# Kernel optimization log

Hardware: AMD Instinct MI355X
Metric: run time of the kernel (lower is better)

## Reference

```python
import jax, jax.numpy as jnp
import numpy as np

NO = 16          # config['Max_Object']
NT = 8           # config['Max_Time']
FEAT = 512       # config['feat_dims']
VIS_IN = 2048
TGT = 24


def setup_inputs() -> dict:
    key = jax.random.key(0)
    ks = jax.random.split(key, 10)
    b = 16
    N = NT * 2 * NO  # 256
    s = lambda k, *sh: jax.random.normal(k, sh, dtype=jnp.float32) * 0.02
    return {
        "src": jax.random.normal(ks[0], (b, 1, 1, N, VIS_IN), dtype=jnp.float32),
        "tgt_rel": jax.random.randint(ks[1], (b * NT * NO * NO,), 0, TGT, dtype=jnp.int64),
        "w1": s(ks[2], VIS_IN, FEAT), "b1": jnp.zeros((FEAT,), jnp.float32),
        "w2": s(ks[3], FEAT, FEAT),   "b2": jnp.zeros((FEAT,), jnp.float32),
        "wf": s(ks[4], FEAT, FEAT),   "bf": jnp.zeros((FEAT,), jnp.float32),
        "wr": s(ks[5], 2 * FEAT, TGT), "br": jnp.zeros((TGT,), jnp.float32),
    }


def reference(src, tgt_rel, w1, b1, w2, b2, wf, bf, wr, br):
    b = src.shape[0]
    BT = b * NT
    # src[:, 0, 0, :, :] -> (b, N, D) -> (b*NT, 2*NO, D); take visual part [:2048]
    x = src[:, 0, 0, :, :].reshape(BT, 2 * NO, -1)[:, :, :VIS_IN]
    # fc_vis: MLP 2048 -> FEAT -> FEAT
    h = jnp.maximum(x @ w1 + b1, 0.0) @ w2 + b2          # (BT, 2NO, FEAT)
    node_feats = h @ wf + bf                             # fc_fusion
    # vectorized replacement of the NOxNO python double loop:
    # edge[:, i*NO + (j-NO), :] = cat(node[:, i], node[:, j])  for i<NO<=j
    subj = jnp.broadcast_to(node_feats[:, :NO, None, :], (BT, NO, NO, FEAT))
    obj = jnp.broadcast_to(node_feats[:, None, NO:, :], (BT, NO, NO, FEAT))
    edge_feats = jnp.concatenate([subj, obj], axis=-1).reshape(BT, NO * NO, 2 * FEAT)
    out = (edge_feats @ wr + br).reshape(-1, TGT)        # fc_rel
    tgt = tgt_rel.reshape(-1)
    w_cls = jnp.asarray([1.0] + [100.0] * (TGT - 1), dtype=out.dtype)
    logp = jax.nn.log_softmax(out, axis=-1)
    nll = -jnp.take_along_axis(logp, tgt[:, None], axis=1)[:, 0]
    ww = w_cls[tgt]
    loss = jnp.sum(ww * nll) / jnp.sum(ww)  # torch weighted cross_entropy (mean)
    return out, tgt, loss
```

## Files before the change

### kernel.cpp

```cpp
#include <hip/hip_runtime.h>
#include <cstddef>
#include <cstdint>

#define NOBJ   16
#define FEAT   512
#define VIS    2048
#define NTGT   24
#define MROWS  4096
#define EROWS  32768

typedef __attribute__((ext_vector_type(8))) short short8;
typedef __attribute__((ext_vector_type(4))) float f32x4;
typedef __attribute__((ext_vector_type(16))) float f32x16;

__device__ __forceinline__ unsigned short f2bf(float f) {
    union { float f; unsigned int i; } v; v.f = f;
    const unsigned int x = v.i;
    return (unsigned short)((x + 0x7fffu + ((x >> 16) & 1u)) >> 16);
}

__device__ __forceinline__ void gload16(const unsigned short* g, unsigned short* l) {
    __builtin_amdgcn_global_load_lds(
        (const __attribute__((address_space(1))) unsigned int*)(const void*)g,
        (__attribute__((address_space(3))) unsigned int*)(void*)l, 16, 0, 0);
}

__global__ __launch_bounds__(256)
void prep1(const float* __restrict__ w1, unsigned short* __restrict__ w1t,
           const float* __restrict__ wf, const float* __restrict__ bfv,
           const float* __restrict__ wr, float* __restrict__ t1,
           const float* __restrict__ src, unsigned short* __restrict__ srcb,
           float* __restrict__ P) {
    __shared__ float shbuf[FEAT * NTGT];
    const int b   = blockIdx.x;
    const int tid = threadIdx.x;
    if (b < 1024) {
        float (*tile)[33] = (float(*)[33])shbuf;
        const int k0 = (b & 63) * 32;
        const int n0 = (b >> 6) * 32;
        const int tx = tid & 31, ty = tid >> 5;
        #pragma unroll
        for (int r = 0; r < 32; r += 8)
            tile[ty + r][tx] = w1[(size_t)(k0 + ty + r) * FEAT + n0 + tx];
        __syncthreads();
        #pragma unroll
        for (int r = 0; r < 32; r += 8)
            w1t[(size_t)(n0 + ty + r) * VIS + k0 + tx] = f2bf(tile[tx][ty + r]);
    } else if (b < 1050) {
        const int bb = b - 1024;
        const int h  = bb / 13, blk = bb % 13;
        const float* wrh = wr + (size_t)h * FEAT * NTGT;
        for (int idx = tid; idx < FEAT * NTGT; idx += 256)
            shbuf[idx] = wrh[idx];
        __syncthreads();
        if (tid < 252) {
            const int krow = blk * 42 + tid / 6;
            const int cg   = tid % 6;
            if (krow <= 512) {
                const float* rowp = (krow < 512) ? (wf + (size_t)krow * FEAT) : bfv;
                const f32x4* shb4 = (const f32x4*)shbuf;
                f32x4 p = {0.f, 0.f, 0.f, 0.f};
                #pragma unroll 4
                for (int j = 0; j < FEAT; j += 4) {
                    const float4 a = *reinterpret_cast<const float4*>(rowp + j);
                    const f32x4 w0 = shb4[(j + 0) * 6 + cg];
                    const f32x4 w1v = shb4[(j + 1) * 6 + cg];
                    const f32x4 w2v = shb4[(j + 2) * 6 + cg];
                    const f32x4 w3v = shb4[(j + 3) * 6 + cg];
                    p += a.x * w0 + a.y * w1v + a.z * w2v + a.w * w3v;
                }
                *reinterpret_cast<f32x4*>(t1 + ((size_t)h * 513 + krow) * 32 + cg * 4) = p;
            }
        }
    } else if (b < 2074) {
        const int bb = b - 1050;
        #pragma unroll
        for (int q = 0; q < 4; ++q) {
            const size_t i = (size_t)bb * 8192 + q * 2048 + tid * 8;
            const float4 a = *reinterpret_cast<const float4*>(src + i);
            const float4 c = *reinterpret_cast<const float4*>(src + i + 4);
            short8 o;
            o[0] = (short)f2bf(a.x); o[1] = (short)f2bf(a.y);
            o[2] = (short)f2bf(a.z); o[3] = (short)f2bf(a.w);
            o[4] = (short)f2bf(c.x); o[5] = (short)f2bf(c.y);
            o[6] = (short)f2bf(c.z); o[7] = (short)f2bf(c.w);
            *reinterpret_cast<short8*>(srcb + i) = o;
        }
    } else {
        const int bb = b - 2074;
        P[(size_t)bb * 256 + tid] = 0.f;
    }
}

__global__ __launch_bounds__(256)
void prep2(const float* __restrict__ w2, const float* __restrict__ b2,
           const float* __restrict__ t1, unsigned short* __restrict__ wABt,
           float* __restrict__ biasAB) {
    __shared__ float shbuf[FEAT * NTGT];
    const int b   = blockIdx.x;
    const int tid = threadIdx.x;
    const int h   = b / 13, blk = b % 13;
    for (int idx = tid; idx < FEAT * NTGT; idx += 256) {
        const int row = idx / NTGT, col = idx - row * NTGT;
        shbuf[idx] = t1[((size_t)h * 513 + row) * 32 + col];
    }
    __syncthreads();
    if (tid >= 252) return;
    const int r  = blk * 42 + tid / 6;
    const int cg = tid % 6;
    if (r > 512) return;
    const float* rowp = (r < 512) ? (w2 + (size_t)r * FEAT) : b2;
    const f32x4* shb4 = (const f32x4*)shbuf;
    f32x4 p = {0.f, 0.f, 0.f, 0.f};
    #pragma unroll 4
    for (int k = 0; k < FEAT; k += 4) {
        const float4 a = *reinterpret_cast<const float4*>(rowp + k);
        const f32x4 w0 = shb4[(k + 0) * 6 + cg];
        const f32x4 w1v = shb4[(k + 1) * 6 + cg];
        const f32x4 w2v = shb4[(k + 2) * 6 + cg];
        const f32x4 w3v = shb4[(k + 3) * 6 + cg];
        p += a.x * w0 + a.y * w1v + a.z * w2v + a.w * w3v;
    }
    #pragma unroll
    for (int e = 0; e < 4; ++e) {
        const int q = h * NTGT + cg * 4 + e;
        if (r < 512) wABt[(size_t)q * FEAT + r] = f2bf(p[e]);
        else         biasAB[q] = p[e] + t1[((size_t)h * 513 + 512) * 32 + cg * 4 + e];
    }
}

__global__ __launch_bounds__(256)
void gemm1f(const unsigned short* __restrict__ srcb, const unsigned short* __restrict__ w1t,
            const float* __restrict__ b1, const unsigned short* __restrict__ wABt,
            float* __restrict__ P) {
    __shared__ __align__(16) unsigned short As[3][128 * 64];
    __shared__ __align__(16) unsigned short Bs[3][32 * 64];

    const int bid = blockIdx.x;
    const int xcd = bid & 7;
    const int k8  = bid >> 3;
    const int xb  = k8 & 15;
    const int yb  = (xcd << 2) | (k8 >> 4);
    const int m0 = yb * 128;
    const int n0 = xb * 32;

    const int tid  = threadIdx.x;
    const int lane = tid & 63;
    const int wid  = tid >> 6;

    const int aRow = tid >> 3, aCd = (tid & 7) ^ (aRow & 7);
    const int bN   = tid >> 3, bCd = (tid & 7) ^ (bN & 7);
    const size_t aOff = (size_t)(m0 + aRow) * VIS + (aCd << 3);
    const size_t bOff = (size_t)(n0 + bN) * VIS + (bCd << 3);
    const int ldsWb = (wid * 64) << 3;

    f32x16 acc = {};

    #define STAGE(tt, bi)                                                        \
        do {                                                                     \
            const int kn_ = (tt) * 64;                                           \
            _Pragma("unroll")                                                    \
            for (int q_ = 0; q_ < 4; ++q_)                                       \
                gload16(srcb + aOff + (size_t)q_ * 32 * VIS + kn_,               \
                        &As[bi][(q_ * 256) * 8 + ldsWb]);                        \
            gload16(w1t + bOff + kn_, &Bs[bi][ldsWb]);                           \
        } while (0)

    STAGE(0, 0);
    STAGE(1, 1);

    const int NT = VIS / 64;
    for (int t = 0; t < NT; ++t) {
        if (t < NT - 1) asm volatile("s_waitcnt vmcnt(5)" ::: "memory");
        else            asm volatile("s_waitcnt vmcnt(0)" ::: "memory");
        __builtin_amdgcn_s_barrier();
        asm volatile("" ::: "memory");
        if (t + 2 < NT) STAGE(t + 2, (t + 2) % 3);
        const int cb = t % 3;
        #pragma unroll
        for (int k2 = 0; k2 < 4; ++k2) {
            const int chunk = (k2 << 1) + (lane >> 5);
            short8 af, bf8;
            {
                const int row = wid * 32 + (lane & 31);
                const int cw  = chunk ^ (row & 7);
                af = *reinterpret_cast<const short8*>(&As[cb][(row << 6) + (cw << 3)]);
            }
            {
                const int n  = lane & 31;
                const int cw = chunk ^ (n & 7);
                bf8 = *reinterpret_cast<const short8*>(&Bs[cb][(n << 6) + (cw << 3)]);
            }
            acc = __builtin_amdgcn_mfma_f32_32x32x16_bf16(af, bf8, acc, 0, 0, 0);
        }
    }
    #undef STAGE

    unsigned short* Ht = &As[0][0];
    {
        const float bias = b1[n0 + (lane & 31)];
        #pragma unroll
        for (int r = 0; r < 16; ++r) {
            const int row = wid * 32 + (r & 3) + ((r >> 2) << 3) + ((lane >> 5) << 2);
            const float v = fmaxf(acc[r] + bias, 0.f);
            Ht[row * 40 + (lane & 31)] = f2bf(v);
        }
    }
    __syncthreads();

    short8 bq[3];
    #pragma unroll
    for (int t3 = 0; t3 < 3; ++t3)
        bq[t3] = *reinterpret_cast<const short8*>(
            wABt + (size_t)(t3 * 16 + (lane & 15)) * FEAT + n0 + ((lane >> 4) << 3));

    const f32x4 pz = {0.f, 0.f, 0.f, 0.f};
    #pragma unroll
    for (int fr = 0; fr < 2; ++fr) {
        short8 aep;
        {
            const int m = wid * 32 + fr * 16 + (lane & 15);
            aep = *reinterpret_cast<const short8*>(&Ht[m * 40 + ((lane >> 4) << 3)]);
        }
        #pragma unroll
        for (int t3 = 0; t3 < 3; ++t3) {
            f32x4 pp = __builtin_amdgcn_mfma_f32_16x16x32_bf16(aep, bq[t3], pz, 0, 0, 0);
            const int q  = t3 * 16 + (lane & 15);
            const int mb = m0 + wid * 32 + fr * 16 + ((lane >> 4) << 2);
            #pragma unroll
            for (int r = 0; r < 4; ++r)
                atomicAdd(&P[(size_t)(mb + r) * 64 + q], pp[r]);
        }
    }
}

__global__ __launch_bounds__(256)
void out_loss_kernel(const float* __restrict__ P, const float* __restrict__ br,
                     const float* __restrict__ biasAB, const int* __restrict__ tgt,
                     float* __restrict__ out, float* __restrict__ out_tgt,
                     float* __restrict__ partials) {
    __shared__ float sm[32][49];
    const int bt  = blockIdx.x;
    const int tid = threadIdx.x;
    for (int idx = tid; idx < 32 * 48; idx += 256) {
        const int row = idx / 48, col = idx - row * 48;
        sm[row][col] = P[(size_t)(bt * 32 + row) * 64 + col];
    }
    __syncthreads();

    const int r  = bt * 256 + tid;
    const int i  = tid >> 4, j = tid & 15;
    const int tg = tgt[r];

    float vals[NTGT];
    float mx = -1e30f, vtg = 0.f;
    #pragma unroll
    for (int t = 0; t < NTGT; ++t) {
        const float cv = br[t] + biasAB[t] + biasAB[24 + t];
        const float v  = sm[i][t] + sm[16 + j][24 + t] + cv;
        vals[t] = v;
        mx = fmaxf(mx, v);
        if (t == tg) vtg = v;
    }
    float se = 0.f;
    #pragma unroll
    for (int t = 0; t < NTGT; ++t) se += expf(vals[t] - mx);
    const float lse = mx + logf(se);

    float4* o4 = reinterpret_cast<float4*>(out + (size_t)r * NTGT);
    #pragma unroll
    for (int q = 0; q < 6; ++q)
        o4[q] = make_float4(vals[q * 4], vals[q * 4 + 1], vals[q * 4 + 2], vals[q * 4 + 3]);
    out_tgt[r] = (float)tg;

    const float wcl = (tg == 0) ? 1.f : 100.f;
    float p1 = wcl * (lse - vtg);
    float p2 = wcl;
    #pragma unroll
    for (int off = 32; off > 0; off >>= 1) {
        p1 += __shfl_down(p1, off);
        p2 += __shfl_down(p2, off);
    }
    __shared__ float s1[4], s2[4];
    const int lane = tid & 63, wv = tid >> 6;
    if (lane == 0) { s1[wv] = p1; s2[wv] = p2; }
    __syncthreads();
    if (tid == 0) {
        partials[bt]       = s1[0] + s1[1] + s1[2] + s1[3];
        partials[128 + bt] = s2[0] + s2[1] + s2[2] + s2[3];
    }
}

__global__ void final_loss(const float* __restrict__ partials, float* __restrict__ loss) {
    const int t = threadIdx.x;
    float a = partials[t] + partials[t + 64];
    float b = partials[128 + t] + partials[192 + t];
    #pragma unroll
    for (int off = 32; off > 0; off >>= 1) {
        a += __shfl_down(a, off);
        b += __shfl_down(b, off);
    }
    if (t == 0) loss[0] = a / b;
}

extern "C" void kernel_launch(void* const* d_in, const int* in_sizes, int n_in,
                              void* d_out, int out_size, void* d_ws, size_t ws_size,
                              hipStream_t stream) {
    const float* src = (const float*)d_in[0];
    const int*   tgt = (const int*)d_in[1];
    const float* w1  = (const float*)d_in[2];
    const float* b1  = (const float*)d_in[3];
    const float* w2  = (const float*)d_in[4];
    const float* b2  = (const float*)d_in[5];
    const float* wf  = (const float*)d_in[6];
    const float* bfv = (const float*)d_in[7];
    const float* wr  = (const float*)d_in[8];
    const float* br  = (const float*)d_in[9];

    float* ws = (float*)d_ws;
    unsigned short* w1t   = (unsigned short*)(ws);
    unsigned short* srcb  = (unsigned short*)(ws + 524288);
    float*          t1    = ws + 4718592;
    unsigned short* wABt  = (unsigned short*)(ws + 4751424);
    float*          biasAB = ws + 4763712;
    float*          P     = ws + 4763776;
    float*          parts = ws + 5025920;

    float* out_logits = (float*)d_out;
    float* out_tgt    = out_logits + (size_t)EROWS * NTGT;
    float* out_lossp  = out_tgt + EROWS;

    prep1<<<3098, 256, 0, stream>>>(w1, w1t, wf, bfv, wr, t1, src, srcb, P);
    prep2<<<26, 256, 0, stream>>>(w2, b2, t1, wABt, biasAB);
    gemm1f<<<512, 256, 0, stream>>>(srcb, w1t, b1, wABt, P);
    out_loss_kernel<<<128, 256, 0, stream>>>(P, br, biasAB, tgt,
                                             out_logits, out_tgt, parts);
    final_loss<<<1, 64, 0, stream>>>(parts, out_lossp);
}
```

Before: 160.2 us.

## Replace atomic P accumulation with per-panel partial buffers reduced in loss kernel

Each gemm1f block now writes its projected partial sums into its own panel slot of a larger buffer instead of doing atomicAdd into a shared P array. The out_loss kernel sums the 16 panels per element. This removes the zero-init blocks in prep1 and the atomic contention. The MFMA accumulation is also split into two independent accumulators to shorten the dependency chain. The cost is a workspace about 12x larger and more reads in the loss kernel.

```diff
diff --git a/kernel.cpp b/kernel.cpp
--- a/kernel.cpp
+++ b/kernel.cpp
@@ -8,6 +8,7 @@
 #define NTGT   24
 #define MROWS  4096
 #define EROWS  32768
+#define NPAN   16
 
 typedef __attribute__((ext_vector_type(8))) short short8;
 typedef __attribute__((ext_vector_type(4))) float f32x4;
@@ -29,8 +30,7 @@
 void prep1(const float* __restrict__ w1, unsigned short* __restrict__ w1t,
            const float* __restrict__ wf, const float* __restrict__ bfv,
            const float* __restrict__ wr, float* __restrict__ t1,
-           const float* __restrict__ src, unsigned short* __restrict__ srcb,
-           float* __restrict__ P) {
+           const float* __restrict__ src, unsigned short* __restrict__ srcb) {
     __shared__ float shbuf[FEAT * NTGT];
     const int b   = blockIdx.x;
     const int tid = threadIdx.x;
@@ -72,7 +72,7 @@
                 *reinterpret_cast<f32x4*>(t1 + ((size_t)h * 513 + krow) * 32 + cg * 4) = p;
             }
         }
-    } else if (b < 2074) {
+    } else {
         const int bb = b - 1050;
         #pragma unroll
         for (int q = 0; q < 4; ++q) {
@@ -86,9 +86,6 @@
             o[6] = (short)f2bf(c.z); o[7] = (short)f2bf(c.w);
             *reinterpret_cast<short8*>(srcb + i) = o;
         }
-    } else {
-        const int bb = b - 2074;
-        P[(size_t)bb * 256 + tid] = 0.f;
     }
 }
 
@@ -132,7 +129,7 @@
 __global__ __launch_bounds__(256)
 void gemm1f(const unsigned short* __restrict__ srcb, const unsigned short* __restrict__ w1t,
             const float* __restrict__ b1, const unsigned short* __restrict__ wABt,
-            float* __restrict__ P) {
+            float* __restrict__ Ppart) {
     __shared__ __align__(16) unsigned short As[3][128 * 64];
     __shared__ __align__(16) unsigned short Bs[3][32 * 64];
 
@@ -154,7 +151,7 @@
     const size_t bOff = (size_t)(n0 + bN) * VIS + (bCd << 3);
     const int ldsWb = (wid * 64) << 3;
 
-    f32x16 acc = {};
+    f32x16 acc0 = {}, acc1 = {};
 
     #define STAGE(tt, bi)                                                        \
         do {                                                                     \
@@ -191,10 +188,12 @@
                 const int cw = chunk ^ (n & 7);
                 bf8 = *reinterpret_cast<const short8*>(&Bs[cb][(n << 6) + (cw << 3)]);
             }
-            acc = __builtin_amdgcn_mfma_f32_32x32x16_bf16(af, bf8, acc, 0, 0, 0);
+            if (k2 < 2) acc0 = __builtin_amdgcn_mfma_f32_32x32x16_bf16(af, bf8, acc0, 0, 0, 0);
+            else        acc1 = __builtin_amdgcn_mfma_f32_32x32x16_bf16(af, bf8, acc1, 0, 0, 0);
         }
     }
     #undef STAGE
+    acc0 += acc1;
 
     unsigned short* Ht = &As[0][0];
     {
@@ -202,7 +201,7 @@
         #pragma unroll
         for (int r = 0; r < 16; ++r) {
             const int row = wid * 32 + (r & 3) + ((r >> 2) << 3) + ((lane >> 5) << 2);
-            const float v = fmaxf(acc[r] + bias, 0.f);
+            const float v = fmaxf(acc0[r] + bias, 0.f);
             Ht[row * 40 + (lane & 31)] = f2bf(v);
         }
     }
@@ -229,22 +228,27 @@
             const int mb = m0 + wid * 32 + fr * 16 + ((lane >> 4) << 2);
             #pragma unroll
             for (int r = 0; r < 4; ++r)
-                atomicAdd(&P[(size_t)(mb + r) * 64 + q], pp[r]);
+                Ppart[(size_t)(mb + r) * (NPAN * 48) + xb * 48 + q] = pp[r];
         }
     }
 }
 
 __global__ __launch_bounds__(256)
-void out_loss_kernel(const float* __restrict__ P, const float* __restrict__ br,
+void out_loss_kernel(const float* __restrict__ Ppart, const float* __restrict__ br,
                      const float* __restrict__ biasAB, const int* __restrict__ tgt,
                      float* __restrict__ out, float* __restrict__ out_tgt,
                      float* __restrict__ partials) {
     __shared__ float sm[32][49];
     const int bt  = blockIdx.x;
     const int tid = threadIdx.x;
+    const float* Pp = Ppart + (size_t)bt * 32 * (NPAN * 48);
     for (int idx = tid; idx < 32 * 48; idx += 256) {
         const int row = idx / 48, col = idx - row * 48;
-        sm[row][col] = P[(size_t)(bt * 32 + row) * 64 + col];
+        const float* rp = Pp + (size_t)row * (NPAN * 48) + col;
+        float s = 0.f;
+        #pragma unroll
+        for (int p = 0; p < NPAN; ++p) s += rp[p * 48];
+        sm[row][col] = s;
     }
     __syncthreads();
 
@@ -323,17 +327,17 @@
     float*          t1    = ws + 4718592;
     unsigned short* wABt  = (unsigned short*)(ws + 4751424);
     float*          biasAB = ws + 4763712;
-    float*          P     = ws + 4763776;
-    float*          parts = ws + 5025920;
+    float*          Ppart = ws + 4763776;
+    float*          parts = ws + 7909504;
 
     float* out_logits = (float*)d_out;
     float* out_tgt    = out_logits + (size_t)EROWS * NTGT;
     float* out_lossp  = out_tgt + EROWS;
 
-    prep1<<<3098, 256, 0, stream>>>(w1, w1t, wf, bfv, wr, t1, src, srcb, P);
+    prep1<<<2074, 256, 0, stream>>>(w1, w1t, wf, bfv, wr, t1, src, srcb);
     prep2<<<26, 256, 0, stream>>>(w2, b2, t1, wABt, biasAB);
-    gemm1f<<<512, 256, 0, stream>>>(srcb, w1t, b1, wABt, P);
-    out_loss_kernel<<<128, 256, 0, stream>>>(P, br, biasAB, tgt,
+    gemm1f<<<512, 256, 0, stream>>>(srcb, w1t, b1, wABt, Ppart);
+    out_loss_kernel<<<128, 256, 0, stream>>>(Ppart, br, biasAB, tgt,
                                              out_logits, out_tgt, parts);
     final_loss<<<1, 64, 0, stream>>>(parts, out_lossp);
 }
```

Measured after the change: 152.6 us. 1.05x faster.
